# Optimization experiments

Hardware: AMD Instinct MI355X
Metric: run time of the kernel (lower is better)

The kernel has to match this reference:

```python
import jax, jax.numpy as jnp
import numpy as np

D_MODEL = 1024
NUM_HEADS = 16
D_K = D_MODEL // NUM_HEADS
SCALE = D_K ** 0.5


def setup_inputs() -> dict:
    key = jax.random.key(0)
    ks = jax.random.split(key, 11)
    B, S = 2, 2048
    std = 1.0 / np.sqrt(D_MODEL)
    inp = {
        "query": jax.random.normal(ks[0], (B, S, D_MODEL), dtype=jnp.float32),
        "key": jax.random.normal(ks[1], (B, S, D_MODEL), dtype=jnp.float32),
        "value": jax.random.normal(ks[2], (B, S, D_MODEL), dtype=jnp.float32),
        "wq": jax.random.uniform(ks[3], (D_MODEL, D_MODEL), jnp.float32, -std, std),
        "bq": jax.random.uniform(ks[4], (D_MODEL,), jnp.float32, -std, std),
        "wk": jax.random.uniform(ks[5], (D_MODEL, D_MODEL), jnp.float32, -std, std),
        "bk": jax.random.uniform(ks[6], (D_MODEL,), jnp.float32, -std, std),
        "wv": jax.random.uniform(ks[7], (D_MODEL, D_MODEL), jnp.float32, -std, std),
        "bv": jax.random.uniform(ks[8], (D_MODEL,), jnp.float32, -std, std),
        "wo": jax.random.uniform(ks[9], (D_MODEL, D_MODEL), jnp.float32, -std, std),
        "bo": jax.random.uniform(ks[10], (D_MODEL,), jnp.float32, -std, std),
    }
    return inp


def _split_heads(x):
    # [B, S, d_model] -> [B, H, S, d_k]
    B, S, _ = x.shape
    return x.reshape(B, S, NUM_HEADS, D_K).transpose(0, 2, 1, 3)


def reference(query, key, value, wq, bq, wk, bk, wv, bv, wo, bo):
    # Linear layers: torch Linear computes x @ W^T + b; weights here stored as [out, in]
    q = _split_heads(query @ wq.T + bq)  # [B, H, S, d_k]
    k = _split_heads(key @ wk.T + bk)
    v = _split_heads(value @ wv.T + bv)
    scores = jnp.einsum("bhqd,bhkd->bhqk", q, k) / SCALE  # [B, H, Sq, Sk]
    attn = jax.nn.softmax(scores, axis=-1)
    ctx = jnp.einsum("bhqk,bhkd->bhqd", attn, v)  # [B, H, S, d_k]
    B, H, S, dk = ctx.shape
    ctx = ctx.transpose(0, 2, 1, 3).reshape(B, S, D_MODEL)
    return ctx @ wo.T + bo
```

## Files before the change

### kernel.cpp

```cpp
#include <hip/hip_runtime.h>
#include <hip/hip_bf16.h>


typedef __attribute__((ext_vector_type(8))) short short8;
typedef __attribute__((ext_vector_type(4))) float floatx4;

#define D_MODEL 1024
#define SEQ 2048
#define NTOK 4096
#define DK 64
#define NH 16
#define MAT 4194304
#define WMAT 1048576

static __device__ __forceinline__ unsigned short f2bf(float f) {
    unsigned int x = __float_as_uint(f);
    unsigned int r = x + 0x7fffu + ((x >> 16) & 1u);
    return (unsigned short)(r >> 16);
}
static __device__ __forceinline__ float bf2f(unsigned short u) {
    return __uint_as_float(((unsigned int)u) << 16);
}
static __device__ __forceinline__ unsigned pk2(float x, float y) {
    __hip_bfloat162 h = __float22bfloat162_rn(make_float2(x, y));
    return *reinterpret_cast<unsigned*>(&h);
}
static __device__ __forceinline__ short8 cvt8(float4 f0, float4 f1) {
    union { unsigned u[4]; short8 s; } r;
    r.u[0] = pk2(f0.x, f0.y); r.u[1] = pk2(f0.z, f0.w);
    r.u[2] = pk2(f1.x, f1.y); r.u[3] = pk2(f1.z, f1.w);
    return r.s;
}
static __device__ __forceinline__ int permtok(int t) {
    return ((t >> 2) & 3) * 16 + ((t >> 4) & 3) * 4 + (t & 3);
}

__global__ __launch_bounds__(256) void cvt7(
    const float* __restrict__ s0, const float* __restrict__ s1,
    const float* __restrict__ s2, const float* __restrict__ s3,
    const float* __restrict__ s4, const float* __restrict__ s5,
    const float* __restrict__ s6, unsigned short* __restrict__ dst) {
    const float* s; size_t doff; int n;
    switch (blockIdx.y) {
        case 0: s = s0; doff = 0;                          n = MAT;  break;
        case 1: s = s1; doff = (size_t)MAT;                n = MAT;  break;
        case 2: s = s2; doff = (size_t)2 * MAT;            n = MAT;  break;
        case 3: s = s3; doff = (size_t)3 * MAT;            n = WMAT; break;
        case 4: s = s4; doff = (size_t)3 * MAT + WMAT;     n = WMAT; break;
        case 5: s = s5; doff = (size_t)3 * MAT + 2 * WMAT; n = WMAT; break;
        default: s = s6; doff = (size_t)3 * MAT + 3 * WMAT; n = WMAT; break;
    }
    int idx = (blockIdx.x * 256 + threadIdx.x) * 8;
    if (idx >= n) return;
    float4 a = *(const float4*)(s + idx);
    float4 b = *(const float4*)(s + idx + 4);
    *(short8*)&dst[doff + idx] = cvt8(a, b);
}

template <bool F32OUT, bool ROWBIAS, bool PERMN, int OSTRIDE>
static __device__ __forceinline__ void gemm_bb(const unsigned short* __restrict__ X,
                                               const unsigned short* __restrict__ W,
                                               const float* __restrict__ bias,
                                               void* __restrict__ outp) {
    __shared__ __align__(16) unsigned short Asm[128 * 64];
    __shared__ __align__(16) unsigned short Bsm[128 * 64];

    const int tid = threadIdx.x;
    const int lane = tid & 63;
    const int wv = tid >> 6;
    const int g = lane >> 4;
    const int lm = lane & 15;
    const int wr = wv >> 1;
    const int wc = wv & 1;
    const int m0 = blockIdx.y * 128;
    const int n0 = blockIdx.x * 128;
    const int rs = (lm & 7) << 3;

    floatx4 acc[4][4];
#pragma unroll
    for (int mi = 0; mi < 4; ++mi)
#pragma unroll
        for (int ni = 0; ni < 4; ++ni)
            acc[mi][ni] = (floatx4){0.f, 0.f, 0.f, 0.f};

    for (int k0 = 0; k0 < 1024; k0 += 64) {
#pragma unroll
        for (int i = 0; i < 4; ++i) {
            int idx = tid + i * 256;
            int row = idx >> 3;
            int col = (idx & 7) << 3;
            int sc = col ^ ((row & 7) << 3);
            *(uint4*)&Asm[row * 64 + sc] =
                *(const uint4*)&X[(size_t)(m0 + row) * 1024 + k0 + col];
            *(uint4*)&Bsm[row * 64 + sc] =
                *(const uint4*)&W[(size_t)(n0 + row) * 1024 + k0 + col];
        }
        __syncthreads();
#pragma unroll
        for (int ks = 0; ks < 64; ks += 32) {
            short8 af[4], bfr[4];
#pragma unroll
            for (int mi = 0; mi < 4; ++mi)
                af[mi] = *(const short8*)&Asm[(wr * 64 + mi * 16 + lm) * 64 +
                                              ((ks + g * 8) ^ rs)];
#pragma unroll
            for (int ni = 0; ni < 4; ++ni)
                bfr[ni] = *(const short8*)&Bsm[(wc * 64 + ni * 16 + lm) * 64 +
                                               ((ks + g * 8) ^ rs)];
#pragma unroll
            for (int mi = 0; mi < 4; ++mi)
#pragma unroll
                for (int ni = 0; ni < 4; ++ni)
                    acc[mi][ni] = __builtin_amdgcn_mfma_f32_16x16x32_bf16(
                        af[mi], bfr[ni], acc[mi][ni], 0, 0, 0);
        }
        __syncthreads();
    }

    float cb[4];
#pragma unroll
    for (int ni = 0; ni < 4; ++ni)
        cb[ni] = ROWBIAS ? 0.f : bias[n0 + wc * 64 + ni * 16 + lm];
#pragma unroll
    for (int mi = 0; mi < 4; ++mi)
#pragma unroll
        for (int r = 0; r < 4; ++r) {
            int rowg = m0 + wr * 64 + mi * 16 + g * 4 + r;
            float rb = ROWBIAS ? bias[rowg] : 0.f;
#pragma unroll
            for (int ni = 0; ni < 4; ++ni) {
                int colg = n0 + wc * 64 + ni * 16 + lm;
                if (PERMN) colg = (colg & ~63) | permtok(colg & 63);
                float val = acc[mi][ni][r] + (ROWBIAS ? rb : cb[ni]);
                if (F32OUT)
                    ((float*)outp)[(size_t)rowg * OSTRIDE + colg] = val;
                else
                    ((unsigned short*)outp)[(size_t)rowg * OSTRIDE + colg] = f2bf(val);
            }
        }
}

__global__ __launch_bounds__(256) void qkv_gemm_b(
    const unsigned short* __restrict__ Xb, const unsigned short* __restrict__ Wb,
    const float* __restrict__ bq, const float* __restrict__ bk,
    unsigned short* __restrict__ QK) {
    const int z = blockIdx.z;
    const float* bias = (z == 0) ? bq : bk;
    gemm_bb<false, false, false, 1024>(Xb + (size_t)z * MAT, Wb + (size_t)z * WMAT,
                                       bias, QK + (size_t)z * MAT);
}

__global__ __launch_bounds__(256) void vt_gemm_b(
    const unsigned short* __restrict__ Wv, const unsigned short* __restrict__ Xv,
    const float* __restrict__ bv, unsigned short* __restrict__ VT) {
    gemm_bb<false, true, true, 4096>(Wv, Xv, bv, VT);
}

__global__ __launch_bounds__(256) void out_gemm_b(
    const unsigned short* __restrict__ ctx, const unsigned short* __restrict__ Wo,
    const float* __restrict__ bo, float* __restrict__ out) {
    gemm_bb<true, false, false, 1024>(ctx, Wo, bo, out);
}

template <bool ROWBIAS, bool PERMN, int OSTRIDE>
static __device__ __forceinline__ void gemm128_f(const float* __restrict__ X,
                                                 const float* __restrict__ W,
                                                 const float* __restrict__ bias,
                                                 unsigned short* __restrict__ out) {
    __shared__ __align__(16) unsigned short Asm[128 * 72];
    __shared__ __align__(16) unsigned short Bsm[128 * 72];
    const int tid = threadIdx.x;
    const int lane = tid & 63;
    const int wv = tid >> 6;
    const int g = lane >> 4;
    const int lm = lane & 15;
    const int wr = wv >> 1;
    const int wc = wv & 1;
    const int m0 = blockIdx.y * 128;
    const int n0 = blockIdx.x * 128;
    floatx4 acc[4][4];
#pragma unroll
    for (int mi = 0; mi < 4; ++mi)
#pragma unroll
        for (int ni = 0; ni < 4; ++ni)
            acc[mi][ni] = (floatx4){0.f, 0.f, 0.f, 0.f};
    for (int k0 = 0; k0 < 1024; k0 += 64) {
#pragma unroll
        for (int i = 0; i < 4; ++i) {
            int idx = tid + i * 256;
            int row = idx >> 3;
            int col = (idx & 7) << 3;
            const float* sa = &X[(size_t)(m0 + row) * 1024 + k0 + col];
            *(short8*)&Asm[row * 72 + col] = cvt8(*(const float4*)sa, *(const float4*)(sa + 4));
            const float* sb = &W[(size_t)(n0 + row) * 1024 + k0 + col];
            *(short8*)&Bsm[row * 72 + col] = cvt8(*(const float4*)sb, *(const float4*)(sb + 4));
        }
        __syncthreads();
#pragma unroll
        for (int ks = 0; ks < 64; ks += 32) {
            short8 af[4], bfr[4];
#pragma unroll
            for (int mi = 0; mi < 4; ++mi)
                af[mi] = *(const short8*)&Asm[(wr * 64 + mi * 16 + lm) * 72 + ks + g * 8];
#pragma unroll
            for (int ni = 0; ni < 4; ++ni)
                bfr[ni] = *(const short8*)&Bsm[(wc * 64 + ni * 16 + lm) * 72 + ks + g * 8];
#pragma unroll
            for (int mi = 0; mi < 4; ++mi)
#pragma unroll
                for (int ni = 0; ni < 4; ++ni)
                    acc[mi][ni] = __builtin_amdgcn_mfma_f32_16x16x32_bf16(
                        af[mi], bfr[ni], acc[mi][ni], 0, 0, 0);
        }
        __syncthreads();
    }
    float cb[4];
#pragma unroll
    for (int ni = 0; ni < 4; ++ni)
        cb[ni] = ROWBIAS ? 0.f : bias[n0 + wc * 64 + ni * 16 + lm];
#pragma unroll
    for (int mi = 0; mi < 4; ++mi)
#pragma unroll
        for (int r = 0; r < 4; ++r) {
            int rowg = m0 + wr * 64 + mi * 16 + g * 4 + r;
            float rb = ROWBIAS ? bias[rowg] : 0.f;
#pragma unroll
            for (int ni = 0; ni < 4; ++ni) {
                int colg = n0 + wc * 64 + ni * 16 + lm;
                if (PERMN) colg = (colg & ~63) | permtok(colg & 63);
                out[(size_t)rowg * OSTRIDE + colg] =
                    f2bf(acc[mi][ni][r] + (ROWBIAS ? rb : cb[ni]));
            }
        }
}

__global__ __launch_bounds__(256) void qkv_gemm_f(
    const float* __restrict__ xq, const float* __restrict__ xk,
    const float* __restrict__ wq, const float* __restrict__ wk,
    const float* __restrict__ bq, const float* __restrict__ bk,
    unsigned short* __restrict__ q, unsigned short* __restrict__ k) {
    if (blockIdx.z == 0) gemm128_f<false, false, 1024>(xq, wq, bq, q);
    else                 gemm128_f<false, false, 1024>(xk, wk, bk, k);
}

__global__ __launch_bounds__(256) void vt_gemm_f(
    const float* __restrict__ wv, const float* __restrict__ xv,
    const float* __restrict__ bv, unsigned short* __restrict__ VT) {
    gemm128_f<true, true, 4096>(wv, xv, bv, VT);
}

__global__ __launch_bounds__(256) void out_gemm_f(
    const float* __restrict__ wo, const float* __restrict__ bo,
    const unsigned short* __restrict__ ctx, float* __restrict__ out) {
    __shared__ __align__(16) unsigned short Asm[128 * 72];
    __shared__ __align__(16) unsigned short Bsm[128 * 72];
    const int tid = threadIdx.x;
    const int lane = tid & 63;
    const int wv = tid >> 6;
    const int g = lane >> 4;
    const int lm = lane & 15;
    const int wr = wv >> 1;
    const int wc = wv & 1;
    const int m0 = blockIdx.y * 128;
    const int n0 = blockIdx.x * 128;
    floatx4 acc[4][4];
#pragma unroll
    for (int mi = 0; mi < 4; ++mi)
#pragma unroll
        for (int ni = 0; ni < 4; ++ni)
            acc[mi][ni] = (floatx4){0.f, 0.f, 0.f, 0.f};
    for (int k0 = 0; k0 < 1024; k0 += 64) {
#pragma unroll
        for (int i = 0; i < 4; ++i) {
            int idx = tid + i * 256;
            int row = idx >> 3;
            int col = (idx & 7) << 3;
            *(uint4*)&Asm[row * 72 + col] =
                *(const uint4*)&ctx[(size_t)(m0 + row) * 1024 + k0 + col];
            const float* sb = &wo[(size_t)(n0 + row) * 1024 + k0 + col];
            *(short8*)&Bsm[row * 72 + col] = cvt8(*(const float4*)sb, *(const float4*)(sb + 4));
        }
        __syncthreads();
#pragma unroll
        for (int ks = 0; ks < 64; ks += 32) {
            short8 af[4], bfr[4];
#pragma unroll
            for (int mi = 0; mi < 4; ++mi)
                af[mi] = *(const short8*)&Asm[(wr * 64 + mi * 16 + lm) * 72 + ks + g * 8];
#pragma unroll
            for (int ni = 0; ni < 4; ++ni)
                bfr[ni] = *(const short8*)&Bsm[(wc * 64 + ni * 16 + lm) * 72 + ks + g * 8];
#pragma unroll
            for (int mi = 0; mi < 4; ++mi)
#pragma unroll
                for (int ni = 0; ni < 4; ++ni)
                    acc[mi][ni] = __builtin_amdgcn_mfma_f32_16x16x32_bf16(
                        af[mi], bfr[ni], acc[mi][ni], 0, 0, 0);
        }
        __syncthreads();
    }
    float bb[4];
#pragma unroll
    for (int ni = 0; ni < 4; ++ni)
        bb[ni] = bo[n0 + wc * 64 + ni * 16 + lm];
#pragma unroll
    for (int mi = 0; mi < 4; ++mi)
#pragma unroll
        for (int ni = 0; ni < 4; ++ni)
#pragma unroll
            for (int r = 0; r < 4; ++r) {
                int rowg = m0 + wr * 64 + mi * 16 + g * 4 + r;
                int colg = n0 + wc * 64 + ni * 16 + lm;
                out[(size_t)rowg * 1024 + colg] = acc[mi][ni][r] + bb[ni];
            }
}

__global__ __launch_bounds__(256) void attn_kernel(
    const unsigned short* __restrict__ Q, const unsigned short* __restrict__ K,
    const unsigned short* __restrict__ VT, unsigned short* __restrict__ CTX) {
    __shared__ __align__(16) unsigned short Ksm[64 * 64];
    __shared__ __align__(16) unsigned short Vt[64 * 64];

    const int tid = threadIdx.x;
    const int lane = tid & 63;
    const int w = tid >> 6;
    const int g = lane >> 4;
    const int lm = lane & 15;
    const int bh = blockIdx.x;
    const int qt = blockIdx.y;
    const int b = bh >> 4;
    const int h = bh & 15;

    const size_t base = (size_t)b * SEQ * D_MODEL + (size_t)h * DK;
    const size_t vtbase = (size_t)(h * 64) * NTOK + (size_t)b * SEQ;

    const int srow0 = tid >> 3;
    const int scol = (tid & 7) << 3;
    const int swz = scol ^ ((srow0 & 7) << 3);
    const int rs = (lm & 7) << 3;

    short8 qf[2][2];
#pragma unroll
    for (int qs = 0; qs < 2; ++qs) {
        const int qrow = qt * 128 + w * 32 + qs * 16 + lm;
#pragma unroll
        for (int t = 0; t < 2; ++t) {
            short8 raw = *(const short8*)&Q[base + (size_t)qrow * D_MODEL + t * 32 + g * 8];
            union { unsigned u[4]; short8 s; } r;
#pragma unroll
            for (int j = 0; j < 4; ++j) {
                float lo = bf2f((unsigned short)raw[2 * j]) * 0.125f;
                float hi = bf2f((unsigned short)raw[2 * j + 1]) * 0.125f;
                r.u[j] = pk2(lo, hi);
            }
            qf[qs][t] = r.s;
        }
    }

    float lsum[2] = {0.f, 0.f};
    floatx4 Oacc[2][4];
#pragma unroll
    for (int qs = 0; qs < 2; ++qs)
#pragma unroll
        for (int nb = 0; nb < 4; ++nb) Oacc[qs][nb] = (floatx4){0.f, 0.f, 0.f, 0.f};

    for (int kt = 0; kt < SEQ / 64; ++kt) {
        const int krow0 = kt * 64;
#pragma unroll
        for (int i = 0; i < 2; ++i) {
            int row = srow0 + i * 32;
            *(uint4*)&Ksm[row * 64 + swz] =
                *(const uint4*)&K[base + (size_t)(krow0 + row) * D_MODEL + scol];
            *(uint4*)&Vt[row * 64 + swz] =
                *(const uint4*)&VT[vtbase + (size_t)row * NTOK + krow0 + scol];
        }
        __syncthreads();

        float p[2][4][4];
#pragma unroll
        for (int kb = 0; kb < 4; ++kb) {
            short8 ak0 = *(const short8*)&Ksm[(kb * 16 + lm) * 64 + ((0 + g * 8) ^ rs)];
            short8 ak1 = *(const short8*)&Ksm[(kb * 16 + lm) * 64 + ((32 + g * 8) ^ rs)];
#pragma unroll
            for (int qs = 0; qs < 2; ++qs) {
                floatx4 a = (floatx4){0.f, 0.f, 0.f, 0.f};
                a = __builtin_amdgcn_mfma_f32_16x16x32_bf16(ak0, qf[qs][0], a, 0, 0, 0);
                a = __builtin_amdgcn_mfma_f32_16x16x32_bf16(ak1, qf[qs][1], a, 0, 0, 0);
#pragma unroll
                for (int r = 0; r < 4; ++r) p[qs][kb][r] = __expf(a[r]);
                lsum[qs] += (p[qs][kb][0] + p[qs][kb][1]) + (p[qs][kb][2] + p[qs][kb][3]);
            }
        }

#pragma unroll
        for (int cp = 0; cp < 2; ++cp) {
            const int c0 = 2 * cp, c1 = 2 * cp + 1;
            union { unsigned u[4]; short8 s; } ap[2];
#pragma unroll
            for (int qs = 0; qs < 2; ++qs) {
                ap[qs].u[0] = pk2(p[qs][c0][0], p[qs][c0][1]);
                ap[qs].u[1] = pk2(p[qs][c0][2], p[qs][c0][3]);
                ap[qs].u[2] = pk2(p[qs][c1][0], p[qs][c1][1]);
                ap[qs].u[3] = pk2(p[qs][c1][2], p[qs][c1][3]);
            }
#pragma unroll
            for (int nb = 0; nb < 4; ++nb) {
                const int d = nb * 16 + lm;
                short8 bv = *(const short8*)&Vt[d * 64 + ((g * 16 + cp * 8) ^ rs)];
                Oacc[0][nb] = __builtin_amdgcn_mfma_f32_16x16x32_bf16(
                    ap[0].s, bv, Oacc[0][nb], 0, 0, 0);
                Oacc[1][nb] = __builtin_amdgcn_mfma_f32_16x16x32_bf16(
                    ap[1].s, bv, Oacc[1][nb], 0, 0, 0);
            }
        }
        __syncthreads();
    }

#pragma unroll
    for (int qs = 0; qs < 2; ++qs) {
        float l = lsum[qs];
        l += __shfl_xor(l, 16, 64);
        l += __shfl_xor(l, 32, 64);
        float lr[4];
#pragma unroll
        for (int r = 0; r < 4; ++r)
            lr[r] = __shfl(l, g * 4 + r, 64);
#pragma unroll
        for (int nb = 0; nb < 4; ++nb) {
#pragma unroll
            for (int r = 0; r < 4; ++r) {
                float val = Oacc[qs][nb][r] / lr[r];
                int srow = qt * 128 + w * 32 + qs * 16 + g * 4 + r;
                CTX[base + (size_t)srow * D_MODEL + nb * 16 + lm] = f2bf(val);
            }
        }
    }
}

extern "C" void kernel_launch(void* const* d_in, const int* in_sizes, int n_in,
                              void* d_out, int out_size, void* d_ws, size_t ws_size,
                              hipStream_t stream) {
    const float* xq = (const float*)d_in[0];
    const float* xk = (const float*)d_in[1];
    const float* xv = (const float*)d_in[2];
    const float* wq = (const float*)d_in[3];
    const float* bq = (const float*)d_in[4];
    const float* wk = (const float*)d_in[5];
    const float* bk = (const float*)d_in[6];
    const float* wv = (const float*)d_in[7];
    const float* bv = (const float*)d_in[8];
    const float* wo = (const float*)d_in[9];
    const float* bo = (const float*)d_in[10];
    float* out = (float*)d_out;

    unsigned short* ws = (unsigned short*)d_ws;

    if (ws_size >= (size_t)68 * 1024 * 1024) {
        unsigned short* Xb = ws;
        unsigned short* Wb = ws + (size_t)3 * MAT;
        unsigned short* Qw = Wb + (size_t)4 * WMAT;
        unsigned short* Kw = Qw + (size_t)MAT;
        unsigned short* VTw = Kw + (size_t)MAT;
        unsigned short* Cw = VTw + (size_t)MAT;

        cvt7<<<dim3(2048, 7), 256, 0, stream>>>(xq, xk, xv, wq, wk, wv, wo, ws);
        qkv_gemm_b<<<dim3(8, 32, 2), 256, 0, stream>>>(Xb, Wb, bq, bk, Qw);
        vt_gemm_b<<<dim3(32, 8), 256, 0, stream>>>(
            Wb + (size_t)2 * WMAT, Xb + (size_t)2 * MAT, bv, VTw);
        attn_kernel<<<dim3(2 * NH, SEQ / 128), 256, 0, stream>>>(Qw, Kw, VTw, Cw);
        out_gemm_b<<<dim3(8, 32), 256, 0, stream>>>(Cw, Wb + (size_t)3 * WMAT, bo, out);
    } else {
        unsigned short* Qw = ws;
        unsigned short* Kw = ws + (size_t)MAT;
        unsigned short* VTw = ws + (size_t)2 * MAT;
        unsigned short* Cw = ws + (size_t)3 * MAT;
        qkv_gemm_f<<<dim3(8, 32, 2), 256, 0, stream>>>(xq, xk, wq, wk, bq, bk, Qw, Kw);
        vt_gemm_f<<<dim3(32, 8), 256, 0, stream>>>(wv, xv, bv, VTw);
        attn_kernel<<<dim3(2 * NH, SEQ / 128), 256, 0, stream>>>(Qw, Kw, VTw, Cw);
        out_gemm_f<<<dim3(8, 32), 256, 0, stream>>>(wo, bo, Cw, out);
    }
}
```

Before: 246.0 us.

## Double-buffer GEMM and attention tiles with direct global-to-LDS async loads

Replaces register-staged global-to-shared copies with global_load_lds direct-to-LDS loads and double-buffers the shared tiles, so the next K-tile is fetched while the current one is computed. This drops one barrier per iteration. The attention kernel now stages 128 keys per barrier instead of 64. The V^T and output GEMMs use a 64-row M tile to launch twice as many blocks for better CU occupancy. The cost is doubled LDS use, and correctness now depends on the async load swizzle layout and wave-level addressing.

```diff
diff --git a/kernel.cpp b/kernel.cpp
--- a/kernel.cpp
+++ b/kernel.cpp
@@ -33,6 +33,11 @@
 }
 static __device__ __forceinline__ int permtok(int t) {
     return ((t >> 2) & 3) * 16 + ((t >> 4) & 3) * 4 + (t & 3);
+}
+static __device__ __forceinline__ void glds16(const unsigned short* g, unsigned short* l) {
+    __builtin_amdgcn_global_load_lds(
+        (const __attribute__((address_space(1))) void*)g,
+        (__attribute__((address_space(3))) void*)l, 16, 0, 0);
 }
 
 __global__ __launch_bounds__(256) void cvt7(
@@ -57,13 +62,15 @@
     *(short8*)&dst[doff + idx] = cvt8(a, b);
 }
 
-template <bool F32OUT, bool ROWBIAS, bool PERMN, int OSTRIDE>
+template <bool F32OUT, bool ROWBIAS, bool PERMN, int OSTRIDE, int BM>
 static __device__ __forceinline__ void gemm_bb(const unsigned short* __restrict__ X,
                                                const unsigned short* __restrict__ W,
                                                const float* __restrict__ bias,
                                                void* __restrict__ outp) {
-    __shared__ __align__(16) unsigned short Asm[128 * 64];
-    __shared__ __align__(16) unsigned short Bsm[128 * 64];
+    __shared__ __align__(16) unsigned short Asm[2][BM * 64];
+    __shared__ __align__(16) unsigned short Bsm[2][128 * 64];
+    constexpr int MF = BM / 32;
+    constexpr int HALF = BM / 2;
 
     const int tid = threadIdx.x;
     const int lane = tid & 63;
@@ -72,49 +79,59 @@
     const int lm = lane & 15;
     const int wr = wv >> 1;
     const int wc = wv & 1;
-    const int m0 = blockIdx.y * 128;
+    const int m0 = blockIdx.y * BM;
     const int n0 = blockIdx.x * 128;
     const int rs = (lm & 7) << 3;
-
-    floatx4 acc[4][4];
-#pragma unroll
-    for (int mi = 0; mi < 4; ++mi)
+    const int lr = lane >> 3;
+    const int lc = lane & 7;
+
+    auto issue = [&](int k0, int p) {
+#pragma unroll
+        for (int i = 0; i < BM / 32; ++i) {
+            const int r0 = wv * (BM / 4) + i * 8;
+            const int row = r0 + lr;
+            const int gcol = (lc ^ (row & 7)) << 3;
+            glds16(&X[(size_t)(m0 + row) * 1024 + k0 + gcol], &Asm[p][r0 * 64]);
+        }
+#pragma unroll
+        for (int i = 0; i < 4; ++i) {
+            const int r0 = wv * 32 + i * 8;
+            const int row = r0 + lr;
+            const int gcol = (lc ^ (row & 7)) << 3;
+            glds16(&W[(size_t)(n0 + row) * 1024 + k0 + gcol], &Bsm[p][r0 * 64]);
+        }
+    };
+
+    floatx4 acc[MF][4];
+#pragma unroll
+    for (int mi = 0; mi < MF; ++mi)
 #pragma unroll
         for (int ni = 0; ni < 4; ++ni)
             acc[mi][ni] = (floatx4){0.f, 0.f, 0.f, 0.f};
 
-    for (int k0 = 0; k0 < 1024; k0 += 64) {
-#pragma unroll
-        for (int i = 0; i < 4; ++i) {
-            int idx = tid + i * 256;
-            int row = idx >> 3;
-            int col = (idx & 7) << 3;
-            int sc = col ^ ((row & 7) << 3);
-            *(uint4*)&Asm[row * 64 + sc] =
-                *(const uint4*)&X[(size_t)(m0 + row) * 1024 + k0 + col];
-            *(uint4*)&Bsm[row * 64 + sc] =
-                *(const uint4*)&W[(size_t)(n0 + row) * 1024 + k0 + col];
-        }
+    issue(0, 0);
+    for (int k0 = 0, it = 0; k0 < 1024; k0 += 64, ++it) {
+        const int p = it & 1;
         __syncthreads();
+        if (k0 + 64 < 1024) issue(k0 + 64, p ^ 1);
 #pragma unroll
         for (int ks = 0; ks < 64; ks += 32) {
-            short8 af[4], bfr[4];
-#pragma unroll
-            for (int mi = 0; mi < 4; ++mi)
-                af[mi] = *(const short8*)&Asm[(wr * 64 + mi * 16 + lm) * 64 +
-                                              ((ks + g * 8) ^ rs)];
+            short8 af[MF], bfr[4];
+#pragma unroll
+            for (int mi = 0; mi < MF; ++mi)
+                af[mi] = *(const short8*)&Asm[p][(wr * HALF + mi * 16 + lm) * 64 +
+                                                ((ks + g * 8) ^ rs)];
 #pragma unroll
             for (int ni = 0; ni < 4; ++ni)
-                bfr[ni] = *(const short8*)&Bsm[(wc * 64 + ni * 16 + lm) * 64 +
-                                               ((ks + g * 8) ^ rs)];
-#pragma unroll
-            for (int mi = 0; mi < 4; ++mi)
+                bfr[ni] = *(const short8*)&Bsm[p][(wc * 64 + ni * 16 + lm) * 64 +
+                                                 ((ks + g * 8) ^ rs)];
+#pragma unroll
+            for (int mi = 0; mi < MF; ++mi)
 #pragma unroll
                 for (int ni = 0; ni < 4; ++ni)
                     acc[mi][ni] = __builtin_amdgcn_mfma_f32_16x16x32_bf16(
                         af[mi], bfr[ni], acc[mi][ni], 0, 0, 0);
         }
-        __syncthreads();
     }
 
     float cb[4];
@@ -122,10 +139,10 @@
     for (int ni = 0; ni < 4; ++ni)
         cb[ni] = ROWBIAS ? 0.f : bias[n0 + wc * 64 + ni * 16 + lm];
 #pragma unroll
-    for (int mi = 0; mi < 4; ++mi)
+    for (int mi = 0; mi < MF; ++mi)
 #pragma unroll
         for (int r = 0; r < 4; ++r) {
-            int rowg = m0 + wr * 64 + mi * 16 + g * 4 + r;
+            int rowg = m0 + wr * HALF + mi * 16 + g * 4 + r;
             float rb = ROWBIAS ? bias[rowg] : 0.f;
 #pragma unroll
             for (int ni = 0; ni < 4; ++ni) {
@@ -146,20 +163,20 @@
     unsigned short* __restrict__ QK) {
     const int z = blockIdx.z;
     const float* bias = (z == 0) ? bq : bk;
-    gemm_bb<false, false, false, 1024>(Xb + (size_t)z * MAT, Wb + (size_t)z * WMAT,
-                                       bias, QK + (size_t)z * MAT);
+    gemm_bb<false, false, false, 1024, 128>(Xb + (size_t)z * MAT, Wb + (size_t)z * WMAT,
+                                            bias, QK + (size_t)z * MAT);
 }
 
 __global__ __launch_bounds__(256) void vt_gemm_b(
     const unsigned short* __restrict__ Wv, const unsigned short* __restrict__ Xv,
     const float* __restrict__ bv, unsigned short* __restrict__ VT) {
-    gemm_bb<false, true, true, 4096>(Wv, Xv, bv, VT);
+    gemm_bb<false, true, true, 4096, 64>(Wv, Xv, bv, VT);
 }
 
 __global__ __launch_bounds__(256) void out_gemm_b(
     const unsigned short* __restrict__ ctx, const unsigned short* __restrict__ Wo,
     const float* __restrict__ bo, float* __restrict__ out) {
-    gemm_bb<true, false, false, 1024>(ctx, Wo, bo, out);
+    gemm_bb<true, false, false, 1024, 64>(ctx, Wo, bo, out);
 }
 
 template <bool ROWBIAS, bool PERMN, int OSTRIDE>
@@ -318,8 +335,8 @@
 __global__ __launch_bounds__(256) void attn_kernel(
     const unsigned short* __restrict__ Q, const unsigned short* __restrict__ K,
     const unsigned short* __restrict__ VT, unsigned short* __restrict__ CTX) {
-    __shared__ __align__(16) unsigned short Ksm[64 * 64];
-    __shared__ __align__(16) unsigned short Vt[64 * 64];
+    __shared__ __align__(16) unsigned short Ksm[2][128 * 64];
+    __shared__ __align__(16) unsigned short Vtsm[2][128 * 64];
 
     const int tid = threadIdx.x;
     const int lane = tid & 63;
@@ -333,11 +350,9 @@
 
     const size_t base = (size_t)b * SEQ * D_MODEL + (size_t)h * DK;
     const size_t vtbase = (size_t)(h * 64) * NTOK + (size_t)b * SEQ;
-
-    const int srow0 = tid >> 3;
-    const int scol = (tid & 7) << 3;
-    const int swz = scol ^ ((srow0 & 7) << 3);
     const int rs = (lm & 7) << 3;
+    const int lr = lane >> 3;
+    const int lc = lane & 7;
 
     short8 qf[2][2];
 #pragma unroll
@@ -364,56 +379,70 @@
 #pragma unroll
         for (int nb = 0; nb < 4; ++nb) Oacc[qs][nb] = (floatx4){0.f, 0.f, 0.f, 0.f};
 
-    for (int kt = 0; kt < SEQ / 64; ++kt) {
-        const int krow0 = kt * 64;
-#pragma unroll
-        for (int i = 0; i < 2; ++i) {
-            int row = srow0 + i * 32;
-            *(uint4*)&Ksm[row * 64 + swz] =
-                *(const uint4*)&K[base + (size_t)(krow0 + row) * D_MODEL + scol];
-            *(uint4*)&Vt[row * 64 + swz] =
-                *(const uint4*)&VT[vtbase + (size_t)row * NTOK + krow0 + scol];
-        }
+    auto issue_pair = [&](int pr, int p) {
+        const int krow0 = pr * 128;
+#pragma unroll
+        for (int i = 0; i < 4; ++i) {
+            const int r0 = w * 32 + i * 8;
+            const int row = r0 + lr;
+            const int gcol = (lc ^ (row & 7)) << 3;
+            glds16(&K[base + (size_t)(krow0 + row) * D_MODEL + gcol], &Ksm[p][r0 * 64]);
+            glds16(&VT[vtbase + (size_t)(row & 63) * NTOK + krow0 + (row >> 6) * 64 + gcol],
+                   &Vtsm[p][r0 * 64]);
+        }
+    };
+
+    const int NP = SEQ / 128;
+    issue_pair(0, 0);
+    for (int pr = 0; pr < NP; ++pr) {
+        const int p = pr & 1;
         __syncthreads();
-
-        float p[2][4][4];
-#pragma unroll
-        for (int kb = 0; kb < 4; ++kb) {
-            short8 ak0 = *(const short8*)&Ksm[(kb * 16 + lm) * 64 + ((0 + g * 8) ^ rs)];
-            short8 ak1 = *(const short8*)&Ksm[(kb * 16 + lm) * 64 + ((32 + g * 8) ^ rs)];
-#pragma unroll
-            for (int qs = 0; qs < 2; ++qs) {
-                floatx4 a = (floatx4){0.f, 0.f, 0.f, 0.f};
-                a = __builtin_amdgcn_mfma_f32_16x16x32_bf16(ak0, qf[qs][0], a, 0, 0, 0);
-                a = __builtin_amdgcn_mfma_f32_16x16x32_bf16(ak1, qf[qs][1], a, 0, 0, 0);
-#pragma unroll
-                for (int r = 0; r < 4; ++r) p[qs][kb][r] = __expf(a[r]);
-                lsum[qs] += (p[qs][kb][0] + p[qs][kb][1]) + (p[qs][kb][2] + p[qs][kb][3]);
-            }
-        }
-
-#pragma unroll
-        for (int cp = 0; cp < 2; ++cp) {
-            const int c0 = 2 * cp, c1 = 2 * cp + 1;
-            union { unsigned u[4]; short8 s; } ap[2];
-#pragma unroll
-            for (int qs = 0; qs < 2; ++qs) {
-                ap[qs].u[0] = pk2(p[qs][c0][0], p[qs][c0][1]);
-                ap[qs].u[1] = pk2(p[qs][c0][2], p[qs][c0][3]);
-                ap[qs].u[2] = pk2(p[qs][c1][0], p[qs][c1][1]);
-                ap[qs].u[3] = pk2(p[qs][c1][2], p[qs][c1][3]);
-            }
-#pragma unroll
-            for (int nb = 0; nb < 4; ++nb) {
-                const int d = nb * 16 + lm;
-                short8 bv = *(const short8*)&Vt[d * 64 + ((g * 16 + cp * 8) ^ rs)];
-                Oacc[0][nb] = __builtin_amdgcn_mfma_f32_16x16x32_bf16(
-                    ap[0].s, bv, Oacc[0][nb], 0, 0, 0);
-                Oacc[1][nb] = __builtin_amdgcn_mfma_f32_16x16x32_bf16(
-                    ap[1].s, bv, Oacc[1][nb], 0, 0, 0);
-            }
-        }
-        __syncthreads();
+        if (pr + 1 < NP) issue_pair(pr + 1, p ^ 1);
+
+#pragma unroll
+        for (int s = 0; s < 2; ++s) {
+            const unsigned short* Kt = &Ksm[p][s * 4096];
+            const unsigned short* Vv = &Vtsm[p][s * 4096];
+
+            float pa[2][4][4];
+#pragma unroll
+            for (int kb = 0; kb < 4; ++kb) {
+                short8 ak0 = *(const short8*)&Kt[(kb * 16 + lm) * 64 + ((0 + g * 8) ^ rs)];
+                short8 ak1 = *(const short8*)&Kt[(kb * 16 + lm) * 64 + ((32 + g * 8) ^ rs)];
+#pragma unroll
+                for (int qs = 0; qs < 2; ++qs) {
+                    floatx4 a = (floatx4){0.f, 0.f, 0.f, 0.f};
+                    a = __builtin_amdgcn_mfma_f32_16x16x32_bf16(ak0, qf[qs][0], a, 0, 0, 0);
+                    a = __builtin_amdgcn_mfma_f32_16x16x32_bf16(ak1, qf[qs][1], a, 0, 0, 0);
+#pragma unroll
+                    for (int r = 0; r < 4; ++r) pa[qs][kb][r] = __expf(a[r]);
+                    lsum[qs] += (pa[qs][kb][0] + pa[qs][kb][1]) +
+                                (pa[qs][kb][2] + pa[qs][kb][3]);
+                }
+            }
+
+#pragma unroll
+            for (int cp = 0; cp < 2; ++cp) {
+                const int c0 = 2 * cp, c1 = 2 * cp + 1;
+                union { unsigned u[4]; short8 s; } ap[2];
+#pragma unroll
+                for (int qs = 0; qs < 2; ++qs) {
+                    ap[qs].u[0] = pk2(pa[qs][c0][0], pa[qs][c0][1]);
+                    ap[qs].u[1] = pk2(pa[qs][c0][2], pa[qs][c0][3]);
+                    ap[qs].u[2] = pk2(pa[qs][c1][0], pa[qs][c1][1]);
+                    ap[qs].u[3] = pk2(pa[qs][c1][2], pa[qs][c1][3]);
+                }
+#pragma unroll
+                for (int nb = 0; nb < 4; ++nb) {
+                    const int d = nb * 16 + lm;
+                    short8 bv = *(const short8*)&Vv[d * 64 + ((g * 16 + cp * 8) ^ rs)];
+                    Oacc[0][nb] = __builtin_amdgcn_mfma_f32_16x16x32_bf16(
+                        ap[0].s, bv, Oacc[0][nb], 0, 0, 0);
+                    Oacc[1][nb] = __builtin_amdgcn_mfma_f32_16x16x32_bf16(
+                        ap[1].s, bv, Oacc[1][nb], 0, 0, 0);
+                }
+            }
+        }
     }
 
 #pragma unroll
@@ -421,15 +450,15 @@
         float l = lsum[qs];
         l += __shfl_xor(l, 16, 64);
         l += __shfl_xor(l, 32, 64);
-        float lr[4];
+        float lr4[4];
 #pragma unroll
         for (int r = 0; r < 4; ++r)
-            lr[r] = __shfl(l, g * 4 + r, 64);
+            lr4[r] = __shfl(l, g * 4 + r, 64);
 #pragma unroll
         for (int nb = 0; nb < 4; ++nb) {
 #pragma unroll
             for (int r = 0; r < 4; ++r) {
-                float val = Oacc[qs][nb][r] / lr[r];
+                float val = Oacc[qs][nb][r] / lr4[r];
                 int srow = qt * 128 + w * 32 + qs * 16 + g * 4 + r;
                 CTX[base + (size_t)srow * D_MODEL + nb * 16 + lm] = f2bf(val);
             }
@@ -465,10 +494,10 @@
 
         cvt7<<<dim3(2048, 7), 256, 0, stream>>>(xq, xk, xv, wq, wk, wv, wo, ws);
         qkv_gemm_b<<<dim3(8, 32, 2), 256, 0, stream>>>(Xb, Wb, bq, bk, Qw);
-        vt_gemm_b<<<dim3(32, 8), 256, 0, stream>>>(
+        vt_gemm_b<<<dim3(32, 16), 256, 0, stream>>>(
             Wb + (size_t)2 * WMAT, Xb + (size_t)2 * MAT, bv, VTw);
         attn_kernel<<<dim3(2 * NH, SEQ / 128), 256, 0, stream>>>(Qw, Kw, VTw, Cw);
-        out_gemm_b<<<dim3(8, 32), 256, 0, stream>>>(Cw, Wb + (size_t)3 * WMAT, bo, out);
+        out_gemm_b<<<dim3(8, 64), 256, 0, stream>>>(Cw, Wb + (size_t)3 * WMAT, bo, out);
     } else {
         unsigned short* Qw = ws;
         unsigned short* Kw = ws + (size_t)MAT;
```

Measured after the change: 235.0 us. -4.5%, faster.
